# Optimization experiments

Hardware: AMD Instinct MI355X
Metric: run time of the kernel (lower is better)

## Reference

```python
import jax, jax.numpy as jnp
import numpy as np

H = 16
D_MODEL = 1024
D_K = D_MODEL // H


def setup_inputs() -> dict:
    key = jax.random.key(0)
    ks = jax.random.split(key, 8)
    B, S = 4, 2048
    query = jax.random.normal(ks[0], (B, S, D_MODEL), dtype=jnp.float32)
    key_t = jax.random.normal(ks[1], (B, S, D_MODEL), dtype=jnp.float32)
    value = jax.random.normal(ks[2], (B, S, D_MODEL), dtype=jnp.float32)
    mask = jax.random.randint(ks[3], (B, S, S), 0, 2, dtype=jnp.int32)
    sc = 1.0 / np.sqrt(D_MODEL)
    Wq = jax.random.normal(ks[4], (D_MODEL, D_MODEL), dtype=jnp.float32) * sc
    Wk = jax.random.normal(ks[5], (D_MODEL, D_MODEL), dtype=jnp.float32) * sc
    Wv = jax.random.normal(ks[6], (D_MODEL, D_MODEL), dtype=jnp.float32) * sc
    Wo = jax.random.normal(ks[7], (D_MODEL, D_MODEL), dtype=jnp.float32) * sc
    return {"query": query, "key": key_t, "value": value, "mask": mask,
            "Wq": Wq, "Wk": Wk, "Wv": Wv, "Wo": Wo}


def reference(query, key, value, mask, Wq, Wk, Wv, Wo):
    B, S, _ = query.shape
    # nn.Linear(bias=False): y = x @ W^T; then split heads -> [B,H,S,d_k]
    def proj(x, W):
        return (x @ W.T).reshape(B, S, H, D_K).transpose(0, 2, 1, 3)

    q = proj(query, Wq)
    k = proj(key, Wk)
    v = proj(value, Wv)

    m = (mask[:, None, :, :] != 0)  # [B,1,S,S] broadcast over heads
    scores = jnp.einsum('bhqd,bhkd->bhqk', q, k) / jnp.sqrt(jnp.float32(D_K))
    scores = jnp.where(m, scores, jnp.float32(-1e9))
    p_attn = jax.nn.softmax(scores, axis=-1)
    p_attn = jnp.where(m, p_attn, 0.0)
    # dropout is identity in eval mode
    x = jnp.einsum('bhqk,bhkd->bhqd', p_attn, v)
    x = x.transpose(0, 2, 1, 3).reshape(B, S, D_MODEL)
    return x @ Wo.T
```

## Files before the change

kernel.cpp:

```cpp
#include <hip/hip_runtime.h>


typedef __attribute__((ext_vector_type(8))) short frag8;
typedef __attribute__((ext_vector_type(4))) float f32x4;
typedef unsigned long long ull;

#define MFMA16(a,b,c) __builtin_amdgcn_mfma_f32_16x16x32_bf16((a),(b),(c),0,0,0)

__device__ __forceinline__ short f2bf(float f) {
  union { float f; unsigned u; } x; x.f = f;
  unsigned r = (x.u + 0x7fffu + ((x.u >> 16) & 1u)) >> 16;
  return (short)r;
}

__device__ __forceinline__ unsigned pkbf(float lo, float hi) {
  union { float f; unsigned u; } a, b;
  a.f = lo; b.f = hi;
  return __builtin_amdgcn_perm(b.u + 0x8000u, a.u + 0x8000u, 0x07060302u);
}

__device__ __forceinline__ unsigned pkbf_t(float lo, float hi) {
  union { float f; unsigned u; } a, b;
  a.f = lo; b.f = hi;
  return __builtin_amdgcn_perm(b.u, a.u, 0x07060302u);
}

__device__ __forceinline__ unsigned bit2m(unsigned word, int off) {
  unsigned r;
  asm("v_bfe_i32 %0, %1, %2, 1" : "=v"(r) : "v"(word), "v"(off));
  return r;
}
__device__ __forceinline__ unsigned mk2(unsigned word, int base) {
  return __builtin_amdgcn_perm(bit2m(word, base + 1), bit2m(word, base),
                               0x05040100u);
}

__device__ __forceinline__ void gl16(const void* g, void* l) {
  __builtin_amdgcn_global_load_lds(
      (const __attribute__((address_space(1))) unsigned*)g,
      (__attribute__((address_space(3))) unsigned*)l, 16, 0, 0);
}

__global__ __launch_bounds__(256) void cast_qkv(
    const float* __restrict__ q, const float* __restrict__ k,
    const float* __restrict__ v, short* __restrict__ qo,
    short* __restrict__ ko, short* __restrict__ vo) {
  int z = blockIdx.x >> 13;
  int i = (blockIdx.x & 8191) * 256 + threadIdx.x;
  const float* s = z == 0 ? q : z == 1 ? k : v;
  short* d = z == 0 ? qo : z == 1 ? ko : vo;
  float4 f = ((const float4*)s)[i];
  short4 o;
  o.x = f2bf(f.x); o.y = f2bf(f.y); o.z = f2bf(f.z); o.w = f2bf(f.w);
  ((short4*)d)[i] = o;
}

__global__ __launch_bounds__(256) void cast_w(
    const float* __restrict__ wq, const float* __restrict__ wk,
    const float* __restrict__ wv, const float* __restrict__ wo,
    short* __restrict__ oq, short* __restrict__ ok,
    short* __restrict__ ov, short* __restrict__ oo) {
  int z = blockIdx.x >> 10;
  int i = (blockIdx.x & 1023) * 256 + threadIdx.x;
  const float* s = z == 0 ? wq : z == 1 ? wk : z == 2 ? wv : wo;
  short* d = z == 0 ? oq : z == 1 ? ok : z == 2 ? ov : oo;
  float sc = (z == 0) ? 0.18033688011f : 1.0f;
  float4 f = ((const float4*)s)[i];
  short4 o;
  o.x = f2bf(f.x * sc); o.y = f2bf(f.y * sc);
  o.z = f2bf(f.z * sc); o.w = f2bf(f.w * sc);
  ((short4*)d)[i] = o;
}

__global__ __launch_bounds__(256) void pack_mask(
    const int* __restrict__ mask, ull* __restrict__ bits) {
  int wv = threadIdx.x >> 6, l = threadIdx.x & 63;
  size_t row = (size_t)blockIdx.x * 4 + wv;
  const int* src = mask + row * 2048;
  for (int c = 0; c < 2048; c += 64) {
    ull bl = __ballot(src[c + l] != 0);
    if (l == 0) bits[(size_t)(c >> 6) * 8192 + row] = bl;
  }
}

template <int MODE>
__device__ __forceinline__ void gemm_body(const short* __restrict__ A,
                                          const short* __restrict__ W,
                                          void* __restrict__ outp, int bid) {
  __shared__ short As[2][128 * 32];
  __shared__ short Bs[2][128 * 32];
  const int t = threadIdx.x;
  const int l = t & 63, wv = t >> 6;
  const int lg = l >> 4, lr = l & 15;
  const int wm = (wv >> 1) * 64, wn = (wv & 1) * 64;
  const int m0 = (bid >> 3) * 128;
  const int n0 = (bid & 7) * 128;

  auto stage = [&](int buf, int kt) {
    const int k0 = kt * 32;
#pragma unroll
    for (int c = 0; c < 2; ++c) {
      int idx = c * 256 + t;
      int row = idx >> 2, ch = (idx & 3) * 8;
      gl16(A + (size_t)(m0 + row) * 1024 + k0 + ch, &As[buf][idx * 8]);
      gl16(W + (size_t)(n0 + row) * 1024 + k0 + ch, &Bs[buf][idx * 8]);
    }
  };

  f32x4 acc[4][4] = {};
  stage(0, 0);
  asm volatile("s_waitcnt vmcnt(0)" ::: "memory");
  __syncthreads();
  int buf = 0;
  for (int kt = 0; kt < 32; ++kt) {
    if (kt + 1 < 32) stage(buf ^ 1, kt + 1);
    frag8 af[4], bf[4];
#pragma unroll
    for (int i = 0; i < 4; ++i) {
      af[i] = *(const frag8*)&As[buf][(wm + i * 16 + lr) * 32 + 8 * lg];
      bf[i] = *(const frag8*)&Bs[buf][(wn + i * 16 + lr) * 32 + 8 * lg];
    }
    __builtin_amdgcn_s_setprio(1);
#pragma unroll
    for (int mi = 0; mi < 4; ++mi)
#pragma unroll
      for (int ni = 0; ni < 4; ++ni)
        acc[mi][ni] = MFMA16(af[mi], bf[ni], acc[mi][ni]);
    __builtin_amdgcn_s_setprio(0);
    asm volatile("s_waitcnt vmcnt(0)" ::: "memory");
    __syncthreads();
    buf ^= 1;
  }

#pragma unroll
  for (int mi = 0; mi < 4; ++mi)
#pragma unroll
    for (int ni = 0; ni < 4; ++ni)
#pragma unroll
      for (int r = 0; r < 4; ++r) {
        int m = m0 + wm + mi * 16 + 4 * lg + r;
        int n = n0 + wn + ni * 16 + lr;
        if (MODE == 0) {
          int b = m >> 11, s = m & 2047, h = n >> 6, dk = n & 63;
          ((short*)outp)[(((size_t)b * 16 + h) * 2048 + s) * 64 + dk] =
              f2bf(acc[mi][ni][r]);
        } else {
          ((float*)outp)[(size_t)m * 1024 + n] = acc[mi][ni][r];
        }
      }
}

__global__ __launch_bounds__(256) void gemm_qkv(
    const short* __restrict__ A0, const short* __restrict__ A1,
    const short* __restrict__ A2, const short* __restrict__ W0,
    const short* __restrict__ W1, const short* __restrict__ W2,
    short* __restrict__ O0, short* __restrict__ O1, short* __restrict__ O2) {
  int wg = (blockIdx.x & 7) * 192 + (blockIdx.x >> 3);
  int z = wg >> 9, bid = wg & 511;
  const short* A = z == 0 ? A0 : z == 1 ? A1 : A2;
  const short* W = z == 0 ? W0 : z == 1 ? W1 : W2;
  short* O = z == 0 ? O0 : z == 1 ? O1 : O2;
  gemm_body<0>(A, W, O, bid);
}

__global__ __launch_bounds__(256) void gemm_o(
    const short* __restrict__ A, const short* __restrict__ W,
    float* __restrict__ O) {
  int bid = (blockIdx.x & 7) * 64 + (blockIdx.x >> 3);
  gemm_body<1>(A, W, O, bid);
}

__global__ __launch_bounds__(256) void transpose_v(
    const short* __restrict__ Vp, short* __restrict__ Vt) {
  __shared__ short lds[64 * 72];
  int bh = blockIdx.y, s0 = blockIdx.x * 64;
  int t = threadIdx.x;
  int rr = t >> 3, c0 = (t & 7) * 8;
#pragma unroll
  for (int half = 0; half < 2; ++half) {
    int r = half * 32 + rr;
    frag8 v = *(const frag8*)(Vp + ((size_t)bh * 2048 + s0 + r) * 64 + c0);
#pragma unroll
    for (int j = 0; j < 8; ++j) lds[r * 72 + c0 + j] = v[j];
  }
  __syncthreads();
#pragma unroll
  for (int half = 0; half < 2; ++half) {
    int d = half * 32 + rr;
    frag8 o;
#pragma unroll
    for (int j = 0; j < 8; ++j) o[j] = lds[(c0 + j) * 72 + d];
    *(frag8*)(Vt + ((size_t)bh * 64 + d) * 2048 + s0 + c0) = o;
  }
}

__global__ __launch_bounds__(256, 4) void attn_fwd(
    const short* __restrict__ Qp, const short* __restrict__ Kp,
    const short* __restrict__ Vt, const ull* __restrict__ mb64,
    short* __restrict__ X) {
  __shared__ short Ks[2][64 * 64];
  __shared__ short Vs[2][64 * 64];
  __shared__ short Ps[4][16 * 64];

  const int wg = (blockIdx.x & 7) * 128 + (blockIdx.x >> 3);
  const int qt = wg & 15, bh = wg >> 4;
  const int b = bh >> 4, h = bh & 15;
  const int t = threadIdx.x;
  const int l = t & 63, wv = t >> 6;
  const int lg = l >> 4, lr = l & 15;
  const int q0 = qt * 128 + wv * 32;
  const int qrow_base = b << 11;

  frag8 qf[2][2];
  const short* Qb = Qp + ((size_t)bh * 2048 + q0) * 64;
#pragma unroll
  for (int qb = 0; qb < 2; ++qb)
#pragma unroll
    for (int kc = 0; kc < 2; ++kc)
      qf[qb][kc] = *(const frag8*)(Qb + (qb * 16 + lr) * 64 + kc * 32 + 8 * lg);

  f32x4 acc[4][2] = {};
  f32x4 accl[2] = {};

  const size_t kbase = (size_t)bh * 2048 * 64;
  const size_t vbase = (size_t)bh * 64 * 2048;
  short* Pw = &Ps[wv][0];
  const int sx = lr & 7;

  frag8 ones;
#pragma unroll
  for (int j = 0; j < 8; ++j) ones[j] = (short)0x3F80;

  auto stageK = [&](int buf, int kt) {
#pragma unroll
    for (int p = 0; p < 2; ++p) {
      int idx = p * 256 + t;
      int row = idx >> 3, c = idx & 7;
      int cs = (c ^ (row & 7)) * 8;
      gl16(Kp + kbase + (size_t)(kt * 64 + row) * 64 + cs, &Ks[buf][idx * 8]);
    }
  };
  auto stageV = [&](int buf, int kt) {
#pragma unroll
    for (int p = 0; p < 2; ++p) {
      int idx = p * 256 + t;
      int row = idx >> 3, c = idx & 7;
      int cs = (c ^ (row & 7)) * 8;
      gl16(Vt + vbase + (size_t)row * 2048 + kt * 64 + cs, &Vs[buf][idx * 8]);
    }
  };

  const uint2* mbp = (const uint2*)mb64;
  const int row0 = qrow_base + q0 + lr;
  const int row1 = row0 + 16;
  uint2 mw0 = mbp[row0], mw1 = mbp[row1];

  stageK(0, 0);
  stageV(0, 0);
  asm volatile("s_waitcnt vmcnt(0)" ::: "memory");
  __syncthreads();
  int buf = 0;

  for (int kt = 0; kt < 32; ++kt) {
    uint2 mwc0 = mw0, mwc1 = mw1;
    const int nk = (kt + 1) & 31;
    mw0 = mbp[(size_t)nk * 8192 + row0];
    mw1 = mbp[(size_t)nk * 8192 + row1];
    stageV(buf ^ 1, nk);
    stageK(buf ^ 1, nk);

    f32x4 s[4][2] = {};
    __builtin_amdgcn_s_setprio(1);
#pragma unroll
    for (int nb = 0; nb < 4; ++nb) {
      const int ro = (nb * 16 + lr) * 64;
      frag8 k0 = *(const frag8*)&Ks[buf][ro + ((0 + lg) ^ sx) * 8];
      frag8 k1 = *(const frag8*)&Ks[buf][ro + ((4 + lg) ^ sx) * 8];
#pragma unroll
      for (int qb = 0; qb < 2; ++qb) {
        s[nb][qb] = MFMA16(k0, qf[qb][0], s[nb][qb]);
        s[nb][qb] = MFMA16(k1, qf[qb][1], s[nb][qb]);
      }
    }
    __builtin_amdgcn_s_setprio(0);

    auto softmax_store = [&](int qb, uint2 mwq) {
      const int q64 = lr * 64;
#pragma unroll
      for (int nb = 0; nb < 4; ++nb) {
        unsigned word = (nb & 2) ? mwq.y : mwq.x;
        int base = (nb & 1) * 16 + 4 * lg;
        float e0 = __builtin_amdgcn_exp2f(s[nb][qb][0]);
        float e1 = __builtin_amdgcn_exp2f(s[nb][qb][1]);
        float e2 = __builtin_amdgcn_exp2f(s[nb][qb][2]);
        float e3 = __builtin_amdgcn_exp2f(s[nb][qb][3]);
        uint2 w;
        w.x = pkbf_t(e0, e1) & mk2(word, base);
        w.y = pkbf_t(e2, e3) & mk2(word, base + 2);
        int sw = ((2 * nb + (lg >> 1)) ^ sx) * 8 + 4 * (lg & 1);
        *(uint2*)&Pw[q64 + sw] = w;
      }
    };

    frag8 pf0[2], pf1[2];
    softmax_store(0, mwc0);
#pragma unroll
    for (int kc = 0; kc < 2; ++kc)
      pf0[kc] = *(const frag8*)&Pw[lr * 64 + ((kc * 4 + lg) ^ sx) * 8];
    softmax_store(1, mwc1);
#pragma unroll
    for (int kc = 0; kc < 2; ++kc)
      pf1[kc] = *(const frag8*)&Pw[lr * 64 + ((kc * 4 + lg) ^ sx) * 8];

    __builtin_amdgcn_s_setprio(1);
#pragma unroll
    for (int db = 0; db < 4; ++db) {
      const int ro = (db * 16 + lr) * 64;
      frag8 v0 = *(const frag8*)&Vs[buf][ro + ((0 + lg) ^ sx) * 8];
      frag8 v1 = *(const frag8*)&Vs[buf][ro + ((4 + lg) ^ sx) * 8];
      acc[db][0] = MFMA16(v0, pf0[0], acc[db][0]);
      acc[db][0] = MFMA16(v1, pf0[1], acc[db][0]);
      acc[db][1] = MFMA16(v0, pf1[0], acc[db][1]);
      acc[db][1] = MFMA16(v1, pf1[1], acc[db][1]);
    }
    accl[0] = MFMA16(ones, pf0[0], accl[0]);
    accl[0] = MFMA16(ones, pf0[1], accl[0]);
    accl[1] = MFMA16(ones, pf1[0], accl[1]);
    accl[1] = MFMA16(ones, pf1[1], accl[1]);
    __builtin_amdgcn_s_setprio(0);

    asm volatile("s_waitcnt vmcnt(0)" ::: "memory");
    __syncthreads();
    buf ^= 1;
  }

#pragma unroll
  for (int qb = 0; qb < 2; ++qb) {
    float inv = 1.0f / fmaxf(accl[qb][0], 1e-30f);
    int q = q0 + qb * 16 + lr;
    size_t base = (size_t)(qrow_base + q) * 1024 + h * 64 + 4 * lg;
#pragma unroll
    for (int db = 0; db < 4; ++db) {
      uint2 o;
      o.x = pkbf(acc[db][qb][0] * inv, acc[db][qb][1] * inv);
      o.y = pkbf(acc[db][qb][2] * inv, acc[db][qb][3] * inv);
      *(uint2*)&X[base + db * 16] = o;
    }
  }
}

extern "C" void kernel_launch(void* const* d_in, const int* in_sizes, int n_in,
                              void* d_out, int out_size, void* d_ws,
                              size_t ws_size, hipStream_t stream) {
  const float* q  = (const float*)d_in[0];
  const float* k  = (const float*)d_in[1];
  const float* v  = (const float*)d_in[2];
  const int*  msk = (const int*)d_in[3];
  const float* Wq = (const float*)d_in[4];
  const float* Wk = (const float*)d_in[5];
  const float* Wv = (const float*)d_in[6];
  const float* Wo = (const float*)d_in[7];

  const size_t SZ_T = 16777216;
  const size_t SZ_W = 2097152;
  char* ws = (char*)d_ws;
  short* qb  = (short*)(ws + 0 * SZ_T);
  short* kb  = (short*)(ws + 1 * SZ_T);
  short* vb  = (short*)(ws + 2 * SZ_T);
  short* Qp  = (short*)(ws + 3 * SZ_T);
  short* Kp  = (short*)(ws + 4 * SZ_T);
  short* Vp  = (short*)(ws + 5 * SZ_T);
  short* Vt  = (short*)(ws + 6 * SZ_T);
  short* X   = (short*)(ws + 7 * SZ_T);
  short* wqb = (short*)(ws + 8 * SZ_T);
  short* wkb = (short*)(ws + 8 * SZ_T + 1 * SZ_W);
  short* wvb = (short*)(ws + 8 * SZ_T + 2 * SZ_W);
  short* wob = (short*)(ws + 8 * SZ_T + 3 * SZ_W);
  void*  mb  = (void*)(ws + 8 * SZ_T + 4 * SZ_W);
  if (ws_size < 8 * SZ_T + 5 * SZ_W) return;

  cast_qkv<<<24576, 256, 0, stream>>>(q, k, v, qb, kb, vb);
  cast_w<<<4096, 256, 0, stream>>>(Wq, Wk, Wv, Wo, wqb, wkb, wvb, wob);
  gemm_qkv<<<1536, 256, 0, stream>>>(qb, kb, vb, wqb, wkb, wvb, Qp, Kp, Vp);
  pack_mask<<<2048, 256, 0, stream>>>(msk, (ull*)mb);
  transpose_v<<<dim3(32, 64), 256, 0, stream>>>(Vp, Vt);
  attn_fwd<<<1024, 256, 0, stream>>>(Qp, Kp, Vt, (const ull*)mb, X);
  gemm_o<<<512, 256, 0, stream>>>(X, wob, (float*)d_out);
}
```

Measured before the change: 274.1 us.

## Split each KV tile across two waves per query block with LDS reduction

Attention workgroups grow from 4 to 8 waves. Each pair of waves shares a 32-row query block and splits every 64-key tile in half, so each wave does half the QK and PV MFMAs per tile. Partial output and row-sum accumulators are combined through LDS at the end. The aim is more waves in flight to hide latency and fewer instructions per wave per tile, at the cost of an extra reduction, higher LDS use and register pressure under launch_bounds(512,4).

```diff
diff --git a/kernel.cpp b/kernel.cpp
--- a/kernel.cpp
+++ b/kernel.cpp
@@ -194,13 +194,11 @@
   }
 }
 
-__global__ __launch_bounds__(256, 4) void attn_fwd(
+__global__ __launch_bounds__(512, 4) void attn_fwd(
     const short* __restrict__ Qp, const short* __restrict__ Kp,
     const short* __restrict__ Vt, const ull* __restrict__ mb64,
     short* __restrict__ X) {
-  __shared__ short Ks[2][64 * 64];
-  __shared__ short Vs[2][64 * 64];
-  __shared__ short Ps[4][16 * 64];
+  __shared__ __align__(16) short smem[20480];
 
   const int wg = (blockIdx.x & 7) * 128 + (blockIdx.x >> 3);
   const int qt = wg & 15, bh = wg >> 4;
@@ -208,7 +206,8 @@
   const int t = threadIdx.x;
   const int l = t & 63, wv = t >> 6;
   const int lg = l >> 4, lr = l & 15;
-  const int q0 = qt * 128 + wv * 32;
+  const int pw = wv >> 1, kvh = wv & 1;
+  const int q0 = qt * 128 + pw * 32;
   const int qrow_base = b << 11;
 
   frag8 qf[2][2];
@@ -224,36 +223,30 @@
 
   const size_t kbase = (size_t)bh * 2048 * 64;
   const size_t vbase = (size_t)bh * 64 * 2048;
-  short* Pw = &Ps[wv][0];
+  short* Pw = &smem[16384 + wv * 512];
   const int sx = lr & 7;
+  const int sxp = (lr >> 1) & 3;
 
   frag8 ones;
 #pragma unroll
   for (int j = 0; j < 8; ++j) ones[j] = (short)0x3F80;
 
+  const int srow = t >> 3, sc = t & 7;
+  const int scs = (sc ^ (srow & 7)) * 8;
   auto stageK = [&](int buf, int kt) {
-#pragma unroll
-    for (int p = 0; p < 2; ++p) {
-      int idx = p * 256 + t;
-      int row = idx >> 3, c = idx & 7;
-      int cs = (c ^ (row & 7)) * 8;
-      gl16(Kp + kbase + (size_t)(kt * 64 + row) * 64 + cs, &Ks[buf][idx * 8]);
-    }
+    gl16(Kp + kbase + (size_t)(kt * 64 + srow) * 64 + scs,
+         &smem[buf * 4096 + t * 8]);
   };
   auto stageV = [&](int buf, int kt) {
-#pragma unroll
-    for (int p = 0; p < 2; ++p) {
-      int idx = p * 256 + t;
-      int row = idx >> 3, c = idx & 7;
-      int cs = (c ^ (row & 7)) * 8;
-      gl16(Vt + vbase + (size_t)row * 2048 + kt * 64 + cs, &Vs[buf][idx * 8]);
-    }
+    gl16(Vt + vbase + (size_t)srow * 2048 + kt * 64 + scs,
+         &smem[8192 + buf * 4096 + t * 8]);
   };
 
-  const uint2* mbp = (const uint2*)mb64;
+  const unsigned* mbp32 = (const unsigned*)mb64;
   const int row0 = qrow_base + q0 + lr;
   const int row1 = row0 + 16;
-  uint2 mw0 = mbp[row0], mw1 = mbp[row1];
+  unsigned mw0 = mbp32[(size_t)row0 * 2 + kvh];
+  unsigned mw1 = mbp32[(size_t)row1 * 2 + kvh];
 
   stageK(0, 0);
   stageV(0, 0);
@@ -262,20 +255,21 @@
   int buf = 0;
 
   for (int kt = 0; kt < 32; ++kt) {
-    uint2 mwc0 = mw0, mwc1 = mw1;
+    unsigned mwc0 = mw0, mwc1 = mw1;
     const int nk = (kt + 1) & 31;
-    mw0 = mbp[(size_t)nk * 8192 + row0];
-    mw1 = mbp[(size_t)nk * 8192 + row1];
+    mw0 = mbp32[((size_t)nk * 8192 + row0) * 2 + kvh];
+    mw1 = mbp32[((size_t)nk * 8192 + row1) * 2 + kvh];
     stageV(buf ^ 1, nk);
     stageK(buf ^ 1, nk);
 
-    f32x4 s[4][2] = {};
+    const short* Kb = &smem[buf * 4096];
+    f32x4 s[2][2] = {};
     __builtin_amdgcn_s_setprio(1);
 #pragma unroll
-    for (int nb = 0; nb < 4; ++nb) {
-      const int ro = (nb * 16 + lr) * 64;
-      frag8 k0 = *(const frag8*)&Ks[buf][ro + ((0 + lg) ^ sx) * 8];
-      frag8 k1 = *(const frag8*)&Ks[buf][ro + ((4 + lg) ^ sx) * 8];
+    for (int nb = 0; nb < 2; ++nb) {
+      const int ro = (kvh * 32 + nb * 16 + lr) * 64;
+      frag8 k0 = *(const frag8*)&Kb[ro + ((0 + lg) ^ sx) * 8];
+      frag8 k1 = *(const frag8*)&Kb[ro + ((4 + lg) ^ sx) * 8];
 #pragma unroll
       for (int qb = 0; qb < 2; ++qb) {
         s[nb][qb] = MFMA16(k0, qf[qb][0], s[nb][qb]);
@@ -284,12 +278,11 @@
     }
     __builtin_amdgcn_s_setprio(0);
 
-    auto softmax_store = [&](int qb, uint2 mwq) {
-      const int q64 = lr * 64;
-#pragma unroll
-      for (int nb = 0; nb < 4; ++nb) {
-        unsigned word = (nb & 2) ? mwq.y : mwq.x;
-        int base = (nb & 1) * 16 + 4 * lg;
+    auto softmax_store = [&](int qb, unsigned word) {
+      const int q32 = lr * 32;
+#pragma unroll
+      for (int nb = 0; nb < 2; ++nb) {
+        int base = nb * 16 + 4 * lg;
         float e0 = __builtin_amdgcn_exp2f(s[nb][qb][0]);
         float e1 = __builtin_amdgcn_exp2f(s[nb][qb][1]);
         float e2 = __builtin_amdgcn_exp2f(s[nb][qb][2]);
@@ -297,36 +290,28 @@
         uint2 w;
         w.x = pkbf_t(e0, e1) & mk2(word, base);
         w.y = pkbf_t(e2, e3) & mk2(word, base + 2);
-        int sw = ((2 * nb + (lg >> 1)) ^ sx) * 8 + 4 * (lg & 1);
-        *(uint2*)&Pw[q64 + sw] = w;
+        int sw = ((2 * nb + (lg >> 1)) ^ sxp) * 8 + 4 * (lg & 1);
+        *(uint2*)&Pw[q32 + sw] = w;
       }
     };
 
-    frag8 pf0[2], pf1[2];
+    frag8 pf0, pf1;
     softmax_store(0, mwc0);
-#pragma unroll
-    for (int kc = 0; kc < 2; ++kc)
-      pf0[kc] = *(const frag8*)&Pw[lr * 64 + ((kc * 4 + lg) ^ sx) * 8];
+    pf0 = *(const frag8*)&Pw[lr * 32 + ((lg ^ sxp)) * 8];
     softmax_store(1, mwc1);
-#pragma unroll
-    for (int kc = 0; kc < 2; ++kc)
-      pf1[kc] = *(const frag8*)&Pw[lr * 64 + ((kc * 4 + lg) ^ sx) * 8];
-
+    pf1 = *(const frag8*)&Pw[lr * 32 + ((lg ^ sxp)) * 8];
+
+    const short* Vb = &smem[8192 + buf * 4096];
     __builtin_amdgcn_s_setprio(1);
 #pragma unroll
     for (int db = 0; db < 4; ++db) {
-      const int ro = (db * 16 + lr) * 64;
-      frag8 v0 = *(const frag8*)&Vs[buf][ro + ((0 + lg) ^ sx) * 8];
-      frag8 v1 = *(const frag8*)&Vs[buf][ro + ((4 + lg) ^ sx) * 8];
-      acc[db][0] = MFMA16(v0, pf0[0], acc[db][0]);
-      acc[db][0] = MFMA16(v1, pf0[1], acc[db][0]);
-      acc[db][1] = MFMA16(v0, pf1[0], acc[db][1]);
-      acc[db][1] = MFMA16(v1, pf1[1], acc[db][1]);
-    }
-    accl[0] = MFMA16(ones, pf0[0], accl[0]);
-    accl[0] = MFMA16(ones, pf0[1], accl[0]);
-    accl[1] = MFMA16(ones, pf1[0], accl[1]);
-    accl[1] = MFMA16(ones, pf1[1], accl[1]);
+      frag8 vf = *(const frag8*)&Vb[(db * 16 + lr) * 64 +
+                                    ((kvh * 4 + lg) ^ sx) * 8];
+      acc[db][0] = MFMA16(vf, pf0, acc[db][0]);
+      acc[db][1] = MFMA16(vf, pf1, acc[db][1]);
+    }
+    accl[0] = MFMA16(ones, pf0, accl[0]);
+    accl[1] = MFMA16(ones, pf1, accl[1]);
     __builtin_amdgcn_s_setprio(0);
 
     asm volatile("s_waitcnt vmcnt(0)" ::: "memory");
@@ -334,17 +319,40 @@
     buf ^= 1;
   }
 
-#pragma unroll
-  for (int qb = 0; qb < 2; ++qb) {
-    float inv = 1.0f / fmaxf(accl[qb][0], 1e-30f);
-    int q = q0 + qb * 16 + lr;
-    size_t base = (size_t)(qrow_base + q) * 1024 + h * 64 + 4 * lg;
-#pragma unroll
-    for (int db = 0; db < 4; ++db) {
-      uint2 o;
-      o.x = pkbf(acc[db][qb][0] * inv, acc[db][qb][1] * inv);
-      o.y = pkbf(acc[db][qb][2] * inv, acc[db][qb][3] * inv);
-      *(uint2*)&X[base + db * 16] = o;
+  float* mf = (float*)smem;
+  __syncthreads();
+  if (kvh) {
+#pragma unroll
+    for (int i = 0; i < 8; ++i)
+      *(f32x4*)&mf[pw * 2048 + i * 256 + l * 4] = acc[i >> 1][i & 1];
+#pragma unroll
+    for (int qb = 0; qb < 2; ++qb)
+      *(f32x4*)&mf[8192 + pw * 512 + qb * 256 + l * 4] = accl[qb];
+  }
+  __syncthreads();
+  if (!kvh) {
+#pragma unroll
+    for (int i = 0; i < 8; ++i) {
+      f32x4 p = *(const f32x4*)&mf[pw * 2048 + i * 256 + l * 4];
+      acc[i >> 1][i & 1] += p;
+    }
+#pragma unroll
+    for (int qb = 0; qb < 2; ++qb) {
+      f32x4 p = *(const f32x4*)&mf[8192 + pw * 512 + qb * 256 + l * 4];
+      accl[qb] += p;
+    }
+#pragma unroll
+    for (int qb = 0; qb < 2; ++qb) {
+      float inv = 1.0f / fmaxf(accl[qb][0], 1e-30f);
+      int q = q0 + qb * 16 + lr;
+      size_t base = (size_t)(qrow_base + q) * 1024 + h * 64 + 4 * lg;
+#pragma unroll
+      for (int db = 0; db < 4; ++db) {
+        uint2 o;
+        o.x = pkbf(acc[db][qb][0] * inv, acc[db][qb][1] * inv);
+        o.y = pkbf(acc[db][qb][2] * inv, acc[db][qb][3] * inv);
+        *(uint2*)&X[base + db * 16] = o;
+      }
     }
   }
 }
@@ -384,6 +392,6 @@
   gemm_qkv<<<1536, 256, 0, stream>>>(qb, kb, vb, wqb, wkb, wvb, Qp, Kp, Vp);
   pack_mask<<<2048, 256, 0, stream>>>(msk, (ull*)mb);
   transpose_v<<<dim3(32, 64), 256, 0, stream>>>(Vp, Vt);
-  attn_fwd<<<1024, 256, 0, stream>>>(Qp, Kp, Vt, (const ull*)mb, X);
+  attn_fwd<<<1024, 512, 0, stream>>>(Qp, Kp, Vt, (const ull*)mb, X);
   gemm_o<<<512, 256, 0, stream>>>(X, wob, (float*)d_out);
 }
```

New measurement: 252.9 us. 1.08x faster.
